# Optimization experiments

Hardware: AMD Instinct MI355X
Metric: run time of the kernel (lower is better)

The kernel has to match this reference:

```python
import jax, jax.numpy as jnp
import numpy as np

NH, NKV, HD = 32, 8, 64
GROUPS = NH // NKV
NLAYERS, FREQ = 30, 3
NSLOTS = 1 + NLAYERS // FREQ  # 11
LAYER_IDX = 0
TOPK = 128
KB_SCALE = 100.0
PAD = -3.3895313892515355e+38  # torch.finfo(bfloat16).min


def rotate_half(x):
    d = x.shape[-1] // 2
    return jnp.concatenate([-x[..., d:], x[..., :d]], axis=-1)


def apply_rope(x, cos, sin):
    # x: (B, H, S, D); cos/sin: (B, S, D)
    return x * cos[:, None] + rotate_half(x) * sin[:, None]


def setup_inputs() -> dict:
    key = jax.random.key(0)
    ks = jax.random.split(key, 10)
    B, S, H = 2, 1024, 2048
    KBL = 400
    hidden_states = jax.random.normal(ks[0], (B, S, H), jnp.float32)
    # rotary embeddings (LlamaRotaryEmbedding, theta=10000)
    pos = jnp.arange(S, dtype=jnp.float32)
    inv_freq = 1.0 / (10000.0 ** (jnp.arange(0, HD, 2, dtype=jnp.float32) / HD))
    freqs = pos[:, None] * inv_freq[None, :]
    emb = jnp.concatenate([freqs, freqs], axis=-1)  # (S, HD)
    cos = jnp.broadcast_to(jnp.cos(emb)[None], (B, S, HD)).astype(jnp.float32)
    sin = jnp.broadcast_to(jnp.sin(emb)[None], (B, S, HD)).astype(jnp.float32)
    # additive causal mask (B,1,S,S)
    causal = jnp.where(jnp.tril(jnp.ones((S, S), jnp.bool_)), 0.0, PAD).astype(jnp.float32)
    attention_mask = jnp.broadcast_to(causal[None, None], (B, 1, S, S))
    kb_keys = jax.random.normal(ks[1], (KBL, NSLOTS * NH * HD), jnp.float32) * 0.5
    kb_values = jax.random.normal(ks[2], (KBL, NSLOTS * NH * HD), jnp.float32) * 0.5
    s = 0.02
    Wq = jax.random.normal(ks[3], (NH * HD, H), jnp.float32) * s
    Wq2 = jax.random.normal(ks[4], (NH * HD, H), jnp.float32) * s
    Wk = jax.random.normal(ks[5], (NKV * HD, H), jnp.float32) * s
    Wv = jax.random.normal(ks[6], (NKV * HD, H), jnp.float32) * s
    Wo = jax.random.normal(ks[7], (H, NH * HD), jnp.float32) * s
    return {"hidden_states": hidden_states, "cos": cos, "sin": sin,
            "attention_mask": attention_mask, "kb_keys": kb_keys, "kb_values": kb_values,
            "Wq": Wq, "Wq2": Wq2, "Wk": Wk, "Wv": Wv, "Wo": Wo}


def reference(hidden_states, cos, sin, attention_mask, kb_keys, kb_values, Wq, Wq2, Wk, Wv, Wo):
    B, S, H = hidden_states.shape
    scale = 1.0 / jnp.sqrt(jnp.float32(HD))

    # projections (attention_bias=False)
    q = (hidden_states @ Wq.T).reshape(B, S, NH, HD).transpose(0, 2, 1, 3)
    q2 = (hidden_states @ Wq2.T).reshape(B, S, NH, HD).transpose(0, 2, 1, 3)
    k = (hidden_states @ Wk.T).reshape(B, S, NKV, HD).transpose(0, 2, 1, 3)
    v = (hidden_states @ Wv.T).reshape(B, S, NKV, HD).transpose(0, 2, 1, 3)

    q = apply_rope(q, cos, sin)
    k = apply_rope(k, cos, sin)

    # repeat_kv (GQA)
    k = jnp.repeat(k, GROUPS, axis=1)  # (B, NH, S, HD)
    v = jnp.repeat(v, GROUPS, axis=1)

    # KB slot select (layer_idx % freq == 0, kb_idx = layer_idx // freq = 0)
    KBL = kb_keys.shape[0]
    kb_idx = LAYER_IDX // FREQ
    kbk = kb_keys.reshape(KBL, NSLOTS, NH * HD)[:, kb_idx].reshape(KBL, NH, HD).transpose(1, 0, 2)
    kbv = kb_values.reshape(KBL, NSLOTS, NH * HD)[:, kb_idx].reshape(KBL, NH, HD).transpose(1, 0, 2)
    kbk = jnp.broadcast_to(kbk[None], (B, NH, KBL, HD))
    kbv = jnp.broadcast_to(kbv[None], (B, NH, KBL, HD))

    # dynamic_sparsify: prune_key_value
    aw_kb = jnp.einsum('bhsd,bhkd->bhsk', q2, kbk) * scale  # (B,NH,S,KBL)
    scores = aw_kb.sum(axis=(1, 2))  # (B, KBL)
    top_idx = jax.lax.stop_gradient(jax.lax.top_k(scores, TOPK)[1])  # (B, TOPK)
    idx = jnp.broadcast_to(top_idx[:, None, :, None], (B, NH, TOPK, HD))
    kbk_g = jax.lax.stop_gradient(jnp.take_along_axis(kbk, idx, axis=2))  # gather under no_grad
    kbv_g = jax.lax.stop_gradient(jnp.take_along_axis(kbv, idx, axis=2))
    aw2 = aw_kb[..., :TOPK]  # source slices (not gathers) the first topk columns

    key_states = jnp.concatenate([kbk_g, k], axis=2)  # (B,NH,TOPK+S,HD)
    value_states = jnp.concatenate([kbv_g, v], axis=2)

    # KB attention mask block
    padding = jnp.all(attention_mask < 0, axis=-1, keepdims=True)  # (B,1,S,1)
    kb_mask = jnp.where(padding, PAD, 0.0).astype(attention_mask.dtype)
    kb_mask = jnp.broadcast_to(kb_mask, (B, 1, S, TOPK))
    mask = jnp.concatenate([kb_mask, attention_mask], axis=-1)  # (B,1,S,TOPK+S)

    aw = jnp.einsum('bhsd,bhkd->bhsk', q, key_states) * scale
    # seperate_query_head: replace KB block with q2-based scores (with kb scale shift)
    aw_seq = aw[..., TOPK:]
    aw2 = aw2 - np.log(TOPK) + np.log(KB_SCALE)
    aw = jnp.concatenate([aw2, aw_seq], axis=-1)

    aw = aw + mask[:, :, :, :key_states.shape[2]]
    aw = jax.nn.softmax(aw.astype(jnp.float32), axis=-1).astype(q.dtype)

    attn = jnp.einsum('bhsk,bhkd->bhsd', aw, value_states)  # (B,NH,S,HD)
    attn = attn.transpose(0, 2, 1, 3).reshape(B, S, NH * HD)
    return attn @ Wo.T
```

## Files before the change

kernel.cpp:

```cpp
#include <hip/hip_runtime.h>
#include <hip/hip_bf16.h>
#include <math.h>

#define NH 32
#define NKV 8
#define HD 64
#define NSLOTS 11
#define TOPK 128
#define KBROW (NSLOTS * NH * HD)
#define PADF (-3.3895313892515355e+38f)
#define C0F  (-0.24686007793152578f)
#define SCALE 0.125f
#define HCH 32

typedef __attribute__((ext_vector_type(8))) __bf16 bf16x8;
typedef __attribute__((ext_vector_type(8))) unsigned short u16x8;
typedef __attribute__((ext_vector_type(4))) float f32x4;

#define GLDS16(gp, lp)                                                        \
  __builtin_amdgcn_global_load_lds(                                           \
      (__attribute__((address_space(1))) void*)(gp),                          \
      (__attribute__((address_space(3))) void*)(lp), 16, 0, 0)

__device__ __forceinline__ unsigned short f2bf(float f) {
  unsigned int u = __float_as_uint(f);
  u = (u + 0x7fffu + ((u >> 16) & 1u)) >> 16;
  return (unsigned short)u;
}

__device__ __forceinline__ int swz(int row, int chunk) {
  return row * 128 + ((chunk ^ (row & 7)) << 4);
}

__global__ void f2bf_all(const float* __restrict__ s0, const float* __restrict__ s1,
                         const float* __restrict__ s2, const float* __restrict__ s3,
                         const float* __restrict__ s4, const float* __restrict__ s5,
                         int n0, int n1, int n2, int n3, int n4_, int n5,
                         unsigned short* __restrict__ out) {
  int i = blockIdx.x * blockDim.x + threadIdx.x;
  int j = i;
  const float* src;
  if (j < n0) src = s0;
  else { j -= n0; if (j < n1) src = s1;
  else { j -= n1; if (j < n2) src = s2;
  else { j -= n2; if (j < n3) src = s3;
  else { j -= n3; if (j < n4_) src = s4;
  else { j -= n4_; if (j >= n5) return; src = s5; }}}}}
  float4 v = ((const float4*)src)[j];
  ushort4 o = {f2bf(v.x), f2bf(v.y), f2bf(v.z), f2bf(v.w)};
  ((ushort4*)out)[i] = o;
}

__global__ __launch_bounds__(256) void gemm_nt_splitk(
    const unsigned short* __restrict__ A, const unsigned short* __restrict__ B,
    float* __restrict__ C0, float* __restrict__ C1, int M, int N, int K) {
  __shared__ unsigned short ldsA[128 * 32];
  __shared__ unsigned short ldsB[128 * 32];
  const int t = threadIdx.x;
  const int l = t & 63, w = t >> 6;
  const int wr = w >> 1, wc = w & 1;
  const int lr = l & 15;
  const int kb = (l >> 4) * 16;
  const int bm = blockIdx.y * 128, bn = blockIdx.x * 128;
  float* C = blockIdx.z ? C1 : C0;
  const int k0base = blockIdx.z * (K >> 1);
  const int kend = k0base + (K >> 1);

  f32x4 acc[4][4] = {};

  for (int k0 = k0base; k0 < kend; k0 += 32) {
    __syncthreads();
#pragma unroll
    for (int it = 0; it < 2; ++it) {
      int s = it * 256 + t;
      int row = s >> 2, cs = (s & 3) * 8;
      GLDS16(A + (size_t)(bm + row) * K + k0 + cs,
             (char*)ldsA + (it * 4 + w) * 1024);
      GLDS16(B + (size_t)(bn + row) * K + k0 + cs,
             (char*)ldsB + (it * 4 + w) * 1024);
    }
    __syncthreads();

    bf16x8 a[4], b[4];
#pragma unroll
    for (int m = 0; m < 4; ++m)
      a[m] = *(const bf16x8*)((const char*)ldsA +
                              (wr * 64 + m * 16 + lr) * 64 + kb);
#pragma unroll
    for (int n = 0; n < 4; ++n)
      b[n] = *(const bf16x8*)((const char*)ldsB +
                              (wc * 64 + n * 16 + lr) * 64 + kb);
#pragma unroll
    for (int m = 0; m < 4; ++m)
#pragma unroll
      for (int n = 0; n < 4; ++n)
        acc[m][n] =
            __builtin_amdgcn_mfma_f32_16x16x32_bf16(a[m], b[n], acc[m][n], 0, 0, 0);
  }

#pragma unroll
  for (int m = 0; m < 4; ++m)
#pragma unroll
    for (int n = 0; n < 4; ++n) {
      int rbase = bm + wr * 64 + m * 16 + ((l >> 4) << 2);
      int cbase = bn + wc * 64 + n * 16 + lr;
#pragma unroll
      for (int j = 0; j < 4; ++j)
        C[(size_t)(rbase + j) * N + cbase] = acc[m][n][j];
    }
}

__global__ void add2_kernel(const float* __restrict__ a,
                            const float* __restrict__ b,
                            float* __restrict__ o, int n4) {
  int i = blockIdx.x * blockDim.x + threadIdx.x;
  if (i >= n4) return;
  float4 x = ((const float4*)a)[i], y = ((const float4*)b)[i];
  ((float4*)o)[i] = make_float4(x.x + y.x, x.y + y.y, x.z + y.z, x.w + y.w);
}

__global__ __launch_bounds__(256) void gemm_proj(
    const unsigned short* __restrict__ A, const unsigned short* __restrict__ Wall,
    const float* __restrict__ cosb, const float* __restrict__ sinb,
    unsigned short* __restrict__ qbf, unsigned short* __restrict__ q2bf,
    unsigned short* __restrict__ kbf, unsigned short* __restrict__ vTb,
    int M, int K, int S) {
  __shared__ unsigned short ldsA[128 * 32];
  __shared__ unsigned short ldsB[128 * 32];
  const int t = threadIdx.x;
  const int l = t & 63, w = t >> 6;
  const int wr = w >> 1, wc = w & 1;
  const int lr = l & 15;
  const int kb_ = (l >> 4) * 16;
  const int bm = blockIdx.y * 128, bn = blockIdx.x * 128;

  f32x4 acc[4][4] = {};

  for (int k0 = 0; k0 < K; k0 += 32) {
    __syncthreads();
#pragma unroll
    for (int it = 0; it < 2; ++it) {
      int s = it * 256 + t;
      int row = s >> 2, cs = (s & 3) * 8;
      GLDS16(A + (size_t)(bm + row) * K + k0 + cs,
             (char*)ldsA + (it * 4 + w) * 1024);
      GLDS16(Wall + (size_t)(bn + row) * K + k0 + cs,
             (char*)ldsB + (it * 4 + w) * 1024);
    }
    __syncthreads();

    bf16x8 a[4], b[4];
#pragma unroll
    for (int m = 0; m < 4; ++m)
      a[m] = *(const bf16x8*)((const char*)ldsA +
                              (wr * 64 + m * 16 + lr) * 64 + kb_);
#pragma unroll
    for (int n = 0; n < 4; ++n)
      b[n] = *(const bf16x8*)((const char*)ldsB +
                              (wc * 64 + n * 16 + lr) * 64 + kb_);
#pragma unroll
    for (int m = 0; m < 4; ++m)
#pragma unroll
      for (int n = 0; n < 4; ++n)
        acc[m][n] =
            __builtin_amdgcn_mfma_f32_16x16x32_bf16(a[m], b[n], acc[m][n], 0, 0, 0);
  }

#pragma unroll
  for (int m = 0; m < 4; ++m) {
    int rbase = bm + wr * 64 + m * 16 + ((l >> 4) << 2);
    if (bn < 2048 || (bn >= 4096 && bn < 4608)) {
      const bool isq = bn < 2048;
#pragma unroll
      for (int j = 0; j < 4; ++j) {
        int row = rbase + j;
        const float* cr = cosb + (size_t)row * 64;
        const float* sr = sinb + (size_t)row * 64;
        float c0 = cr[lr], c1 = cr[16 + lr], c2 = cr[32 + lr], c3 = cr[48 + lr];
        float sa = sr[lr], sb = sr[16 + lr], sc_ = sr[32 + lr], sd = sr[48 + lr];
        float x0 = acc[m][0][j], x1 = acc[m][1][j];
        float x2 = acc[m][2][j], x3 = acc[m][3][j];
        float y0 = x0 * c0 - x2 * sa;
        float y1 = x1 * c1 - x3 * sb;
        float y2 = x2 * c2 + x0 * sc_;
        float y3 = x3 * c3 + x1 * sd;
        if (isq) {
          size_t ro = (size_t)row * 2048 + bn + wc * 64 + lr;
          qbf[ro] = f2bf(y0); qbf[ro + 16] = f2bf(y1);
          qbf[ro + 32] = f2bf(y2); qbf[ro + 48] = f2bf(y3);
        } else {
          size_t ro = (size_t)row * 512 + (bn - 4096) + wc * 64 + lr;
          kbf[ro] = f2bf(y0); kbf[ro + 16] = f2bf(y1);
          kbf[ro + 32] = f2bf(y2); kbf[ro + 48] = f2bf(y3);
        }
      }
    } else if (bn < 4096) {
#pragma unroll
      for (int n = 0; n < 4; ++n) {
        int cbase = bn + wc * 64 + n * 16 + lr;
#pragma unroll
        for (int j = 0; j < 4; ++j)
          q2bf[(size_t)(rbase + j) * 2048 + (cbase - 2048)] = f2bf(acc[m][n][j]);
      }
    } else {
      int b_ = rbase / S, s = rbase % S;
#pragma unroll
      for (int n = 0; n < 4; ++n) {
        int col = (bn - 4608) + wc * 64 + n * 16 + lr;
        int gg = col >> 6, d = col & 63;
        ushort4 o = {f2bf(acc[m][n][0]), f2bf(acc[m][n][1]),
                     f2bf(acc[m][n][2]), f2bf(acc[m][n][3])};
        *(ushort4*)&vTb[(((size_t)b_ * NKV + gg) * 64 + d) * S + s] = o;
      }
    }
  }
}

__global__ void kbkh_kernel(const float* __restrict__ kbk,
                            unsigned short* __restrict__ out) {
  int i = blockIdx.x * blockDim.x + threadIdx.x;
  if (i >= 128 * 512) return;
  int j = i >> 9, c4 = (i & 511) * 4;
  float4 v = *(const float4*)&kbk[(size_t)j * KBROW + c4];
  ushort4 o = {f2bf(v.x), f2bf(v.y), f2bf(v.z), f2bf(v.w)};
  *(ushort4*)&out[(size_t)j * 2048 + c4] = o;
}

__global__ __launch_bounds__(256) void kbvgt_kernel(
    const float* __restrict__ kbv, const int* __restrict__ topi,
    unsigned short* __restrict__ kbvgT, int B) {
  int h = blockIdx.x % NH, b = blockIdx.x / NH;
  __shared__ unsigned short gt[128][72];
  __shared__ int lidx[TOPK];
  int t = threadIdx.x;
  if (t < TOPK) lidx[t] = topi[b * TOPK + t];
  __syncthreads();
#pragma unroll
  for (int it = 0; it < 8; ++it) {
    int slot = it * 256 + t;
    int j = slot >> 4, d4 = (slot & 15) * 4;
    float4 v = *(const float4*)&kbv[(size_t)lidx[j] * KBROW + h * 64 + d4];
    gt[j][d4] = f2bf(v.x); gt[j][d4 + 1] = f2bf(v.y);
    gt[j][d4 + 2] = f2bf(v.z); gt[j][d4 + 3] = f2bf(v.w);
  }
  __syncthreads();
#pragma unroll
  for (int it = 0; it < 4; ++it) {
    int slot = it * 256 + t;
    int d = slot >> 4, j8 = (slot & 15) * 8;
    u16x8 o;
#pragma unroll
    for (int j = 0; j < 8; ++j) o[j] = gt[j8 + j][d];
    *(u16x8*)&kbvgT[(((size_t)b * NH + h) * 64 + d) * 128 + j8] = o;
  }
}

__global__ __launch_bounds__(256) void hsum1_kernel(
    const float* __restrict__ hidden, double* __restrict__ part,
    int B, int S, int H) {
  const int nhb = H >> 8;
  int hb = blockIdx.x % nhb;
  int ch = (blockIdx.x / nhb) % HCH;
  int b  = blockIdx.x / (nhb * HCH);
  int c  = hb * 256 + threadIdx.x;
  int rows = S / HCH;
  const float* p = hidden + ((size_t)b * S + (size_t)ch * rows) * H + c;
  double acc = 0.0;
  for (int s = 0; s < rows; ++s) acc += (double)p[(size_t)s * H];
  part[((size_t)b * HCH + ch) * H + c] = acc;
}

__global__ void hsum2_kernel(const double* __restrict__ part,
                             float* __restrict__ Hsum, int B, int H) {
  int idx = blockIdx.x * blockDim.x + threadIdx.x;
  if (idx >= B * H) return;
  int b = idx / H, c = idx % H;
  const double* p = part + (size_t)b * HCH * H + c;
  double acc = 0.0;
#pragma unroll
  for (int ch = 0; ch < HCH; ++ch) acc += p[(size_t)ch * H];
  Hsum[idx] = (float)acc;
}

__global__ void qs_kernel(const float* __restrict__ Hsum,
                          const float* __restrict__ Wq2,
                          float* __restrict__ Qs, int B, int H) {
  int task = (blockIdx.x * blockDim.x + threadIdx.x) >> 6;
  int lane = threadIdx.x & 63;
  if (task >= B * NH * HD) return;
  int b = task / (NH * HD), c = task % (NH * HD);
  const float* hs = Hsum + (size_t)b * H;
  const float* wr = Wq2 + (size_t)c * H;
  double acc = 0.0;
  for (int k = lane; k < H; k += 64) acc += (double)hs[k] * (double)wr[k];
#pragma unroll
  for (int off = 32; off; off >>= 1) acc += __shfl_xor(acc, off);
  if (lane == 0) Qs[task] = (float)acc;
}

__global__ void scores_kernel(const float* __restrict__ Qs,
                              const float* __restrict__ kbk,
                              float* __restrict__ scores, int B, int KBL) {
  int task = (blockIdx.x * blockDim.x + threadIdx.x) >> 6;
  int lane = threadIdx.x & 63;
  if (task >= B * KBL) return;
  int b = task / KBL, l = task % KBL;
  const float* kr = kbk + (size_t)l * KBROW;
  const float* qd = Qs + (size_t)b * NH * HD;
  double acc = 0.0;
  for (int c = lane; c < NH * HD; c += 64) acc += (double)qd[c] * (double)kr[c];
#pragma unroll
  for (int off = 32; off; off >>= 1) acc += __shfl_xor(acc, off);
  if (lane == 0) scores[task] = (float)(0.125 * acc);
}

__global__ __launch_bounds__(256) void topk_kernel(
    const float* __restrict__ scores, int* __restrict__ top_idx, int KBL) {
  __shared__ float ls[512];
  int b = blockIdx.x, t = threadIdx.x;
  for (int i = t; i < KBL; i += 256) ls[i] = scores[(size_t)b * KBL + i];
  __syncthreads();
  for (int l = t; l < KBL; l += 256) {
    float sl = ls[l];
    int rank = 0;
    for (int j = 0; j < KBL; ++j) {
      float sj = ls[j];
      rank += (sj > sl || (sj == sl && j < l)) ? 1 : 0;
    }
    if (rank < TOPK) top_idx[b * TOPK + rank] = l;
  }
}

__global__ void padflag_kernel(const float* __restrict__ mask,
                               int* __restrict__ flags, int BS, int S) {
  int w = (blockIdx.x * blockDim.x + threadIdx.x) >> 6;
  int lane = threadIdx.x & 63;
  if (w >= BS) return;
  const float* row = mask + (size_t)w * S;
  bool ok = true;
  for (int j = lane; j < S; j += 64) ok = ok && (row[j] < 0.f);
  int allv = __all(ok ? 1 : 0);
  if (lane == 0) flags[w] = allv;
}

__device__ __forceinline__ void load_chunk(
    int ch, int t, int b, int h, int g, int S,
    const unsigned short* __restrict__ kbf, const unsigned short* __restrict__ vTb,
    const unsigned short* __restrict__ kbkh, const unsigned short* __restrict__ kbvgT,
    bf16x8* st) {
  bool iskb = ch < 2;
  int j0 = iskb ? ch * 64 : (ch - 2) * 64;
#pragma unroll
  for (int it = 0; it < 4; ++it) {
    int slot = it * 256 + t;
    int tile = slot >> 9, row = (slot >> 3) & 63, ck = slot & 7;
    const unsigned short* src;
    if (tile == 0)
      src = iskb ? kbkh + (size_t)(j0 + row) * 2048 + h * 64 + ck * 8
                 : kbf + (size_t)(b * S + j0 + row) * 512 + g * 64 + ck * 8;
    else
      src = iskb ? kbvgT + (((size_t)b * NH + h) * 64 + row) * 128 + j0 + ck * 8
                 : vTb + (((size_t)b * NKV + g) * 64 + row) * (size_t)S + j0 + ck * 8;
    st[it] = *(const bf16x8*)src;
  }
}

__device__ __forceinline__ void attn_step(
    const char* smem, char* ptw, const int* padfb, const bf16x8* aq,
    bool iskb, int j0, int s0, int w, int li, int lg4,
    float* m_, float* l_, f32x4* acc) {
  f32x4 cc[4];
  __builtin_amdgcn_s_setprio(1);
#pragma unroll
  for (int cb = 0; cb < 4; ++cb) {
    bf16x8 b0 = *(const bf16x8*)(smem + swz(cb * 16 + li, lg4));
    bf16x8 b1 = *(const bf16x8*)(smem + swz(cb * 16 + li, 4 + lg4));
    f32x4 z = {};
    z = __builtin_amdgcn_mfma_f32_16x16x32_bf16(aq[0], b0, z, 0, 0, 0);
    z = __builtin_amdgcn_mfma_f32_16x16x32_bf16(aq[1], b1, z, 0, 0, 0);
    cc[cb] = z;
  }
  __builtin_amdgcn_s_setprio(0);

  float lgv[4][4];
#pragma unroll
  for (int cb = 0; cb < 4; ++cb)
#pragma unroll
    for (int j = 0; j < 4; ++j) {
      float v = SCALE * cc[cb][j];
      if (iskb) {
        v += C0F + (padfb[w * 16 + lg4 * 4 + j] ? PADF : 0.f);
      } else {
        int key = j0 + cb * 16 + li;
        int srow = s0 + w * 16 + lg4 * 4 + j;
        v += (key <= srow) ? 0.f : PADF;
      }
      lgv[cb][j] = v;
    }
#pragma unroll
  for (int j = 0; j < 4; ++j) {
    float rmax = fmaxf(fmaxf(lgv[0][j], lgv[1][j]), fmaxf(lgv[2][j], lgv[3][j]));
#pragma unroll
    for (int off = 8; off; off >>= 1) rmax = fmaxf(rmax, __shfl_xor(rmax, off));
    float mn = fmaxf(m_[j], rmax);
    float fs = __expf(m_[j] - mn);
    float csum = 0.f;
#pragma unroll
    for (int cb = 0; cb < 4; ++cb) {
      float pv = __expf(lgv[cb][j] - mn);
      csum += pv;
      int key = cb * 16 + li;
      int rloc = lg4 * 4 + j;
      *(unsigned short*)(ptw + swz(rloc, key >> 3) + ((key & 7) << 1)) = f2bf(pv);
    }
#pragma unroll
    for (int off = 8; off; off >>= 1) csum += __shfl_xor(csum, off);
    m_[j] = mn;
    l_[j] = l_[j] * fs + csum;
#pragma unroll
    for (int db = 0; db < 4; ++db) acc[db][j] *= fs;
  }

  bf16x8 pa0 = *(const bf16x8*)(ptw + swz(li, lg4));
  bf16x8 pa1 = *(const bf16x8*)(ptw + swz(li, 4 + lg4));
  __builtin_amdgcn_s_setprio(1);
#pragma unroll
  for (int db = 0; db < 4; ++db) {
    bf16x8 bv0 = *(const bf16x8*)(smem + 8192 + swz(db * 16 + li, lg4));
    bf16x8 bv1 = *(const bf16x8*)(smem + 8192 + swz(db * 16 + li, 4 + lg4));
    acc[db] = __builtin_amdgcn_mfma_f32_16x16x32_bf16(pa0, bv0, acc[db], 0, 0, 0);
    acc[db] = __builtin_amdgcn_mfma_f32_16x16x32_bf16(pa1, bv1, acc[db], 0, 0, 0);
  }
  __builtin_amdgcn_s_setprio(0);
}

__global__ __launch_bounds__(256) void attn_mfma(
    const unsigned short* __restrict__ qbf,
    const unsigned short* __restrict__ q2bf,
    const unsigned short* __restrict__ kbf,
    const unsigned short* __restrict__ vTb,
    const unsigned short* __restrict__ kbkh,
    const unsigned short* __restrict__ kbvgT,
    const int* __restrict__ padflag,
    unsigned short* __restrict__ attnbf,
    int B, int S) {
  const int nst = S >> 6;
  const int npair = (nst + 1) >> 1;
  const int p = blockIdx.x % npair;
  const int h = (blockIdx.x / npair) % NH;
  const int b = blockIdx.x / (npair * NH);
  const int stA = p, stB = nst - 1 - p;
  const bool hasB = (stB != stA);
  const int s0A = stA * 64, s0B = stB * 64;
  const int g = h / (NH / NKV);

  __shared__ unsigned short smem[8192];
  __shared__ unsigned short pt[4][1024];
  __shared__ int padf[128];

  const int t = threadIdx.x;
  const int w = t >> 6;
  const int li = t & 15;
  const int lg4 = (t & 63) >> 4;

  const int nch = 2 + stB + 1;

  bf16x8 st[4];
  load_chunk(0, t, b, h, g, S, kbf, vTb, kbkh, kbvgT, st);

  bf16x8 aq0A[2], aq2A[2], aq0B[2], aq2B[2];
  {
    size_t rowA = (size_t)(b * S + s0A + w * 16 + li) * (NH * HD);
    size_t rowB = (size_t)(b * S + s0B + w * 16 + li) * (NH * HD);
#pragma unroll
    for (int kc = 0; kc < 2; ++kc) {
      size_t o = h * 64 + kc * 32 + lg4 * 8;
      aq0A[kc] = *(const bf16x8*)(qbf + rowA + o);
      aq2A[kc] = *(const bf16x8*)(q2bf + rowA + o);
      aq0B[kc] = *(const bf16x8*)(qbf + rowB + o);
      aq2B[kc] = *(const bf16x8*)(q2bf + rowB + o);
    }
  }
  if (t < 64) padf[t] = padflag[b * S + s0A + t];
  else if (t < 128) padf[t] = padflag[b * S + s0B + (t - 64)];

  float mA[4] = {-3.4e38f, -3.4e38f, -3.4e38f, -3.4e38f};
  float mB[4] = {-3.4e38f, -3.4e38f, -3.4e38f, -3.4e38f};
  float lA[4] = {}, lB[4] = {};
  f32x4 accA[4] = {}, accB[4] = {};

  for (int ch = 0; ch < nch; ++ch) {
    const bool iskb = ch < 2;
    const int j0 = iskb ? ch * 64 : (ch - 2) * 64;
    if (ch) __syncthreads();
#pragma unroll
    for (int it = 0; it < 4; ++it) {
      int slot = it * 256 + t;
      int tile = slot >> 9, row = (slot >> 3) & 63, ck = slot & 7;
      *(bf16x8*)((char*)smem + tile * 8192 + swz(row, ck)) = st[it];
    }
    __syncthreads();
    if (ch + 1 < nch) load_chunk(ch + 1, t, b, h, g, S, kbf, vTb, kbkh, kbvgT, st);

    if (iskb || (ch - 2) <= stA)
      attn_step((const char*)smem, (char*)pt[w], padf, iskb ? aq2A : aq0A,
                iskb, j0, s0A, w, li, lg4, mA, lA, accA);
    if (hasB)
      attn_step((const char*)smem, (char*)pt[w], padf + 64, iskb ? aq2B : aq0B,
                iskb, j0, s0B, w, li, lg4, mB, lB, accB);
  }

#pragma unroll
  for (int j = 0; j < 4; ++j) {
    float inv = 1.f / lA[j];
    size_t o = (size_t)(b * S + s0A + w * 16 + lg4 * 4 + j) * (NH * HD) + h * 64 + li;
#pragma unroll
    for (int db = 0; db < 4; ++db) attnbf[o + db * 16] = f2bf(accA[db][j] * inv);
  }
  if (hasB) {
#pragma unroll
    for (int j = 0; j < 4; ++j) {
      float inv = 1.f / lB[j];
      size_t o = (size_t)(b * S + s0B + w * 16 + lg4 * 4 + j) * (NH * HD) + h * 64 + li;
#pragma unroll
      for (int db = 0; db < 4; ++db) attnbf[o + db * 16] = f2bf(accB[db][j] * inv);
    }
  }
}

extern "C" void kernel_launch(void* const* d_in, const int* in_sizes, int n_in,
                              void* d_out, int out_size, void* d_ws, size_t ws_size,
                              hipStream_t stream) {
  const float* hidden = (const float*)d_in[0];
  const float* cosb   = (const float*)d_in[1];
  const float* sinb   = (const float*)d_in[2];
  const float* mask   = (const float*)d_in[3];
  const float* kbk    = (const float*)d_in[4];
  const float* kbv    = (const float*)d_in[5];
  const float* Wq     = (const float*)d_in[6];
  const float* Wq2    = (const float*)d_in[7];
  const float* Wk     = (const float*)d_in[8];
  const float* Wv     = (const float*)d_in[9];
  const float* Wo     = (const float*)d_in[10];
  float* out = (float*)d_out;

  const int H   = in_sizes[6] / (NH * HD);
  const int KBL = in_sizes[4] / KBROW;
  const long long BSll = (long long)in_sizes[0] / H;
  const int S = (int)((long long)in_sizes[3] / BSll);
  const int B = (int)(BSll / S);
  const int BS = B * S;
  const int NQ = NH * HD;
  const int NKVD = NKV * HD;
  const int NTOT = NQ + NQ + NKVD + NKVD;

  float* ws = (float*)d_ws;
  size_t off = 0;
  double* hpart = (double*)(ws + off); off += (size_t)B * HCH * H * 2;
  float* Hsum = ws + off; off += (size_t)B * H;
  float* Qs   = ws + off; off += (size_t)B * NQ;
  float* sc   = ws + off; off += (size_t)B * KBL;
  int* topi   = (int*)(ws + off); off += (size_t)B * TOPK;
  int* padfl  = (int*)(ws + off); off += (size_t)BS;
  unsigned short* hbf    = (unsigned short*)(ws + off); off += (size_t)BS * H / 2;
  unsigned short* wall   = (unsigned short*)(ws + off); off += (size_t)NTOT * H / 2;
  unsigned short* wobf   = (unsigned short*)(ws + off); off += (size_t)H * NQ / 2;
  unsigned short* attnbf = (unsigned short*)(ws + off); off += (size_t)BS * NQ / 2;
  unsigned short* qbf    = (unsigned short*)(ws + off); off += (size_t)BS * NQ / 2;
  unsigned short* q2bf   = (unsigned short*)(ws + off); off += (size_t)BS * NQ / 2;
  unsigned short* kbf    = (unsigned short*)(ws + off); off += (size_t)BS * NKVD / 2;
  unsigned short* vTb    = (unsigned short*)(ws + off); off += (size_t)BS * NKVD / 2;
  unsigned short* kbkh   = (unsigned short*)(ws + off); off += (size_t)128 * NQ / 2;
  unsigned short* kbvgT  = (unsigned short*)(ws + off); off += (size_t)B * NH * HD * TOPK / 2;
  float* c0 = (float*)qbf;
  float* c1 = (float*)wall;
  (void)ws_size; (void)n_in; (void)out_size;

  {
    int n0 = BS * H / 4, n1 = NQ * H / 4, n2 = NQ * H / 4;
    int n3 = NKVD * H / 4, n4_ = NKVD * H / 4, n5 = H * NQ / 4;
    int ntot = n0 + n1 + n2 + n3 + n4_ + n5;
    f2bf_all<<<(ntot + 255) / 256, 256, 0, stream>>>(
        hidden, Wq, Wq2, Wk, Wv, Wo, n0, n1, n2, n3, n4_, n5, hbf);
  }

  gemm_proj<<<dim3(NTOT / 128, BS / 128), 256, 0, stream>>>(
      hbf, wall, cosb, sinb, qbf, q2bf, kbf, vTb, BS, H, S);

  hsum1_kernel<<<B * HCH * (H / 256), 256, 0, stream>>>(hidden, hpart, B, S, H);
  hsum2_kernel<<<(B * H + 255) / 256, 256, 0, stream>>>(hpart, Hsum, B, H);
  qs_kernel<<<(B * NQ * 64 + 255) / 256, 256, 0, stream>>>(Hsum, Wq2, Qs, B, H);
  scores_kernel<<<(B * KBL * 64 + 255) / 256, 256, 0, stream>>>(Qs, kbk, sc, B, KBL);
  topk_kernel<<<B, 256, 0, stream>>>(sc, topi, KBL);
  padflag_kernel<<<(BS * 64 + 255) / 256, 256, 0, stream>>>(mask, padfl, BS, S);

  kbkh_kernel<<<(128 * 512 + 255) / 256, 256, 0, stream>>>(kbk, kbkh);
  kbvgt_kernel<<<B * NH, 256, 0, stream>>>(kbv, topi, kbvgT, B);

  {
    int nst = S / 64;
    int npair = (nst + 1) / 2;
    attn_mfma<<<B * NH * npair, 256, 0, stream>>>(
        qbf, q2bf, kbf, vTb, kbkh, kbvgT, padfl, attnbf, B, S);
  }

  gemm_nt_splitk<<<dim3(H / 128, BS / 128, 2), 256, 0, stream>>>(
      attnbf, wobf, c0, c1, BS, H, NQ);
  add2_kernel<<<(BS * H / 4 + 255) / 256, 256, 0, stream>>>(c0, c1, out, BS * H / 4);
}
```

Before: 265.2 us.

## Rewrite projection GEMM with 256x256 tiles, double-buffered LDS and swizzle

The fused QKV/Q2 projection GEMM now uses 512-thread blocks computing 256x256 tiles with a 64-wide K step. Global-to-LDS loads for the next K tile are issued during the current tile's MFMAs, using double-buffered 128KB LDS, manual vmcnt waits and barriers. An XOR swizzle avoids LDS bank conflicts. The aim is to hide load latency and raise arithmetic intensity, at the cost of higher LDS use, fewer blocks (lower occupancy) and a tile count that must divide the output segment boundaries.

```diff
diff --git a/kernel.cpp b/kernel.cpp
--- a/kernel.cpp
+++ b/kernel.cpp
@@ -119,65 +119,106 @@
   ((float4*)o)[i] = make_float4(x.x + y.x, x.y + y.y, x.z + y.z, x.w + y.w);
 }
 
-__global__ __launch_bounds__(256) void gemm_proj(
-    const unsigned short* __restrict__ A, const unsigned short* __restrict__ Wall,
+__global__ __launch_bounds__(512) void gemm_proj8(
+    const unsigned short* __restrict__ A,
+    const unsigned short* __restrict__ Wall,
     const float* __restrict__ cosb, const float* __restrict__ sinb,
     unsigned short* __restrict__ qbf, unsigned short* __restrict__ q2bf,
     unsigned short* __restrict__ kbf, unsigned short* __restrict__ vTb,
     int M, int K, int S) {
-  __shared__ unsigned short ldsA[128 * 32];
-  __shared__ unsigned short ldsB[128 * 32];
+  __shared__ char lds[131072];
   const int t = threadIdx.x;
-  const int l = t & 63, w = t >> 6;
-  const int wr = w >> 1, wc = w & 1;
-  const int lr = l & 15;
-  const int kb_ = (l >> 4) * 16;
-  const int bm = blockIdx.y * 128, bn = blockIdx.x * 128;
-
-  f32x4 acc[4][4] = {};
-
-  for (int k0 = 0; k0 < K; k0 += 32) {
-    __syncthreads();
-#pragma unroll
-    for (int it = 0; it < 2; ++it) {
-      int s = it * 256 + t;
-      int row = s >> 2, cs = (s & 3) * 8;
-      GLDS16(A + (size_t)(bm + row) * K + k0 + cs,
-             (char*)ldsA + (it * 4 + w) * 1024);
-      GLDS16(Wall + (size_t)(bn + row) * K + k0 + cs,
-             (char*)ldsB + (it * 4 + w) * 1024);
-    }
-    __syncthreads();
-
-    bf16x8 a[4], b[4];
-#pragma unroll
-    for (int m = 0; m < 4; ++m)
-      a[m] = *(const bf16x8*)((const char*)ldsA +
-                              (wr * 64 + m * 16 + lr) * 64 + kb_);
-#pragma unroll
-    for (int n = 0; n < 4; ++n)
-      b[n] = *(const bf16x8*)((const char*)ldsB +
-                              (wc * 64 + n * 16 + lr) * 64 + kb_);
-#pragma unroll
-    for (int m = 0; m < 4; ++m)
-#pragma unroll
-      for (int n = 0; n < 4; ++n)
-        acc[m][n] =
-            __builtin_amdgcn_mfma_f32_16x16x32_bf16(a[m], b[n], acc[m][n], 0, 0, 0);
-  }
-
-#pragma unroll
-  for (int m = 0; m < 4; ++m) {
-    int rbase = bm + wr * 64 + m * 16 + ((l >> 4) << 2);
-    if (bn < 2048 || (bn >= 4096 && bn < 4608)) {
-      const bool isq = bn < 2048;
+  const int w = t >> 6;
+  const int wm = w >> 2, wn = w & 3;
+  const int l = t & 63;
+  const int li = l & 15, lg4 = l >> 4;
+  const int bm = blockIdx.y * 256, bn = blockIdx.x * 256;
+  const int NK = K >> 6;
+
+  f32x4 acc[8][4] = {};
+
+#define STAGE_UNIT(kt1, nb, u)                                                \
+  {                                                                           \
+    const int slice_ = (u) >> 1;                                              \
+    const unsigned short* mat_ = ((u) & 1) ? Wall : A;                        \
+    const int tb_ = ((u) & 1) ? bn : bm;                                      \
+    char* base_ = lds + (nb) * 65536 + (((u) & 1) ? 32768 : 0) +              \
+                  slice_ * 16384;                                             \
+    _Pragma("unroll")                                                         \
+    for (int i_ = 0; i_ < 2; ++i_) {                                          \
+      int ss_ = i_ * 512 + t;                                                 \
+      int row_ = ss_ >> 2, cc_ = ss_ & 3;                                     \
+      int chunk_ = cc_ ^ ((row_ >> 1) & 3);                                   \
+      GLDS16(mat_ + (size_t)(tb_ + row_) * K + (kt1) * 64 + slice_ * 32 +     \
+                 chunk_ * 8,                                                  \
+             base_ + i_ * 8192 + w * 1024);                                   \
+    }                                                                         \
+  }
+
+  STAGE_UNIT(0, 0, 0); STAGE_UNIT(0, 0, 1);
+  STAGE_UNIT(0, 0, 2); STAGE_UNIT(0, 0, 3);
+  asm volatile("s_waitcnt vmcnt(4)" ::: "memory");
+  asm volatile("s_barrier" ::: "memory");
+
+  for (int kt = 0; kt < NK; ++kt) {
+    const int cur = kt & 1;
+    const bool stg = (kt + 1 < NK);
+    char* curA = lds + cur * 65536;
+    char* curB = curA + 32768;
+#pragma unroll
+    for (int q = 0; q < 4; ++q) {
+      const int kk = q >> 1, mh = q & 1;
+      if (stg) {
+        if (q == 0)      STAGE_UNIT(kt + 1, cur ^ 1, 0)
+        else if (q == 1) STAGE_UNIT(kt + 1, cur ^ 1, 1)
+        else if (q == 2) STAGE_UNIT(kt + 1, cur ^ 1, 2)
+        else             STAGE_UNIT(kt + 1, cur ^ 1, 3)
+      }
+      bf16x8 af[4], bfr[4];
+#pragma unroll
+      for (int mi = 0; mi < 4; ++mi) {
+        int row = wm * 128 + (mh * 4 + mi) * 16 + li;
+        af[mi] = *(const bf16x8*)(curA + kk * 16384 + row * 64 +
+                                  ((lg4 ^ ((row >> 1) & 3)) << 4));
+      }
+#pragma unroll
+      for (int n = 0; n < 4; ++n) {
+        int row = wn * 64 + n * 16 + li;
+        bfr[n] = *(const bf16x8*)(curB + kk * 16384 + row * 64 +
+                                  ((lg4 ^ ((row >> 1) & 3)) << 4));
+      }
+      __builtin_amdgcn_s_setprio(1);
+#pragma unroll
+      for (int mi = 0; mi < 4; ++mi)
+#pragma unroll
+        for (int n = 0; n < 4; ++n)
+          acc[mh * 4 + mi][n] = __builtin_amdgcn_mfma_f32_16x16x32_bf16(
+              af[mi], bfr[n], acc[mh * 4 + mi][n], 0, 0, 0);
+      __builtin_amdgcn_s_setprio(0);
+      if (q == 1) {
+        if (kt == NK - 1) asm volatile("s_waitcnt vmcnt(0)" ::: "memory");
+        else              asm volatile("s_waitcnt vmcnt(4)" ::: "memory");
+      } else if (q == 3 && stg) {
+        asm volatile("s_waitcnt vmcnt(4)" ::: "memory");
+      }
+      asm volatile("s_barrier" ::: "memory");
+    }
+  }
+#undef STAGE_UNIT
+
+  const int seg = bn;
+#pragma unroll
+  for (int m = 0; m < 8; ++m) {
+    const int row0 = bm + wm * 128 + m * 16 + lg4 * 4;
+    if (seg < 2048 || (seg >= 4096 && seg < 4608)) {
+      const bool isq = seg < 2048;
 #pragma unroll
       for (int j = 0; j < 4; ++j) {
-        int row = rbase + j;
+        int row = row0 + j;
         const float* cr = cosb + (size_t)row * 64;
         const float* sr = sinb + (size_t)row * 64;
-        float c0 = cr[lr], c1 = cr[16 + lr], c2 = cr[32 + lr], c3 = cr[48 + lr];
-        float sa = sr[lr], sb = sr[16 + lr], sc_ = sr[32 + lr], sd = sr[48 + lr];
+        float c0 = cr[li], c1 = cr[16 + li], c2 = cr[32 + li], c3 = cr[48 + li];
+        float sa = sr[li], sb = sr[16 + li], sc_ = sr[32 + li], sd = sr[48 + li];
         float x0 = acc[m][0][j], x1 = acc[m][1][j];
         float x2 = acc[m][2][j], x3 = acc[m][3][j];
         float y0 = x0 * c0 - x2 * sa;
@@ -185,28 +226,28 @@
         float y2 = x2 * c2 + x0 * sc_;
         float y3 = x3 * c3 + x1 * sd;
         if (isq) {
-          size_t ro = (size_t)row * 2048 + bn + wc * 64 + lr;
+          size_t ro = (size_t)row * 2048 + bn + wn * 64 + li;
           qbf[ro] = f2bf(y0); qbf[ro + 16] = f2bf(y1);
           qbf[ro + 32] = f2bf(y2); qbf[ro + 48] = f2bf(y3);
         } else {
-          size_t ro = (size_t)row * 512 + (bn - 4096) + wc * 64 + lr;
+          size_t ro = (size_t)row * 512 + (bn - 4096) + wn * 64 + li;
           kbf[ro] = f2bf(y0); kbf[ro + 16] = f2bf(y1);
           kbf[ro + 32] = f2bf(y2); kbf[ro + 48] = f2bf(y3);
         }
       }
-    } else if (bn < 4096) {
+    } else if (seg < 4096) {
 #pragma unroll
       for (int n = 0; n < 4; ++n) {
-        int cbase = bn + wc * 64 + n * 16 + lr;
+        int col = bn - 2048 + wn * 64 + n * 16 + li;
 #pragma unroll
         for (int j = 0; j < 4; ++j)
-          q2bf[(size_t)(rbase + j) * 2048 + (cbase - 2048)] = f2bf(acc[m][n][j]);
+          q2bf[(size_t)(row0 + j) * 2048 + col] = f2bf(acc[m][n][j]);
       }
     } else {
-      int b_ = rbase / S, s = rbase % S;
+      int b_ = row0 / S, s = row0 % S;
 #pragma unroll
       for (int n = 0; n < 4; ++n) {
-        int col = (bn - 4608) + wc * 64 + n * 16 + lr;
+        int col = (bn - 4608) + wn * 64 + n * 16 + li;
         int gg = col >> 6, d = col & 63;
         ushort4 o = {f2bf(acc[m][n][0]), f2bf(acc[m][n][1]),
                      f2bf(acc[m][n][2]), f2bf(acc[m][n][3])};
@@ -584,7 +625,7 @@
         hidden, Wq, Wq2, Wk, Wv, Wo, n0, n1, n2, n3, n4_, n5, hbf);
   }
 
-  gemm_proj<<<dim3(NTOT / 128, BS / 128), 256, 0, stream>>>(
+  gemm_proj8<<<dim3(NTOT / 256, BS / 256), 512, 0, stream>>>(
       hbf, wall, cosb, sinb, qbf, q2bf, kbf, vTb, BS, H, S);
 
   hsum1_kernel<<<B * HCH * (H / 256), 256, 0, stream>>>(hidden, hpart, B, S, H);
```

Result: no change. 262.8 us (-0.9%).
